# Kernel optimization log

Hardware: AMD Instinct MI355X
Metric: run time of the kernel (lower is better)

The kernel has to match this reference:

```python
import jax, jax.numpy as jnp
import numpy as np

N_HEAD = 16
N_KV_GROUP = 4
WINDOW = 256


def setup_inputs() -> dict:
    key = jax.random.key(0)
    ks = jax.random.split(key, 5)
    B, T, C = 2, 2048, 1024
    KV = C // N_HEAD * N_KV_GROUP  # 256
    s = 0.02
    return {
        "x": jax.random.normal(ks[0], (B, T, C), jnp.float32),
        "Wq": jax.random.normal(ks[1], (C, C), jnp.float32) * s,
        "bq": jnp.zeros((C,), jnp.float32),
        "Wk": jax.random.normal(ks[2], (C, KV), jnp.float32) * s,
        "bk": jnp.zeros((KV,), jnp.float32),
        "Wv": jax.random.normal(ks[3], (C, KV), jnp.float32) * s,
        "bv": jnp.zeros((KV,), jnp.float32),
        "Wo": jax.random.normal(ks[4], (C, C), jnp.float32) * s,
        "bo": jnp.zeros((C,), jnp.float32),
    }


def reference(x, Wq, bq, Wk, bk, Wv, bv, Wo, bo):
    B, T, C = x.shape
    hd = C // N_HEAD  # head dim = 64
    n_rep = N_HEAD // N_KV_GROUP

    q = x @ Wq + bq                      # [B,T,C]
    k = x @ Wk + bk                      # [B,T,KV]
    v = x @ Wv + bv

    q = q.reshape(B, T, N_HEAD, hd).transpose(0, 2, 1, 3)       # [B,H,T,d]
    k = k.reshape(B, T, N_KV_GROUP, hd).transpose(0, 2, 1, 3)   # [B,G,T,d]
    v = v.reshape(B, T, N_KV_GROUP, hd).transpose(0, 2, 1, 3)

    # GQA: repeat_interleave kv heads along head dim
    k_rep = jnp.repeat(k, n_rep, axis=1)                         # [B,H,T,d]
    v_rep = jnp.repeat(v, n_rep, axis=1)

    att = jnp.einsum("bhqd,bhkd->bhqk", q, k_rep) / jnp.sqrt(jnp.float32(hd))

    # causal + sliding window band mask: q position i attends to j in [i-WINDOW, i]
    i = jnp.arange(T)[:, None]
    j = jnp.arange(T)[None, :]
    band = (j <= i) & (j >= i - WINDOW)                           # [T,T]
    att = jnp.where(band[None, None], att, jnp.float32(-jnp.inf))

    att = jax.nn.softmax(att, axis=-1)
    y = jnp.einsum("bhqk,bhkd->bhqd", att, v_rep)                 # [B,H,T,d]
    y = y.transpose(0, 2, 1, 3).reshape(B, T, C)
    return y @ Wo + bo
```

## Files before the change

### kernel.cpp

```cpp
#include <hip/hip_runtime.h>
#include <hip/hip_bf16.h>

#define TT 2048
#define CC 1024
#define KVD 256
#define QKVD 1536

typedef __bf16 bf16x8 __attribute__((ext_vector_type(8)));
typedef float f32x4 __attribute__((ext_vector_type(4)));

__device__ __forceinline__ void gload_lds16(const __hip_bfloat16* g, __hip_bfloat16* l) {
  __builtin_amdgcn_global_load_lds(
      (const __attribute__((address_space(1))) unsigned int*)g,
      (__attribute__((address_space(3))) unsigned int*)l, 16, 0, 0);
}


__global__ __launch_bounds__(256) void k_prep(const float* __restrict__ x,
                                              const float* __restrict__ Wq,
                                              const float* __restrict__ Wk,
                                              const float* __restrict__ Wv,
                                              const float* __restrict__ Wo,
                                              const float* __restrict__ bq,
                                              const float* __restrict__ bk,
                                              const float* __restrict__ bv,
                                              __hip_bfloat16* __restrict__ xbf,
                                              __hip_bfloat16* __restrict__ wqkvT,
                                              __hip_bfloat16* __restrict__ woT,
                                              float* __restrict__ bqkv) {
  const int bxid = blockIdx.x;
  if (bxid < 4096) {
    size_t idx = ((size_t)bxid * 256 + threadIdx.x) * 4;
    float4 v = *(const float4*)(x + idx);
    xbf[idx + 0] = __float2bfloat16(v.x);
    xbf[idx + 1] = __float2bfloat16(v.y);
    xbf[idx + 2] = __float2bfloat16(v.z);
    xbf[idx + 3] = __float2bfloat16(v.w);
    return;
  }
  if (bxid == 4736) {
    for (int i = threadIdx.x; i < 1536; i += 256) {
      float v;
      if (i < 1024)      v = bq[i];
      else if (i < 1280) v = bk[i - 1024];
      else               v = bv[i - 1280];
      bqkv[i] = v;
    }
    return;
  }
  __shared__ float tile[64][65];
  const float* src;
  int ncols, k0, n0;
  __hip_bfloat16* dst;
  if (bxid < 4480) {
    const int idx = bxid - 4096;
    k0 = (idx & 15) * 64;
    n0 = (idx >> 4) * 64;
    dst = wqkvT;
    if (n0 < 1024)      { src = Wq; ncols = 1024; }
    else if (n0 < 1280) { src = Wk - 1024; ncols = 256; }
    else                { src = Wv - 1280; ncols = 256; }
  } else {
    const int idx = bxid - 4480;
    k0 = (idx & 15) * 64;
    n0 = (idx >> 4) * 64;
    dst = woT; src = Wo; ncols = 1024;
  }
  const int rw = threadIdx.x >> 6;
  const int cl = threadIdx.x & 63;
#pragma unroll
  for (int i = 0; i < 16; ++i) {
    const int kr = rw + i * 4;
    tile[kr][cl] = src[(size_t)(k0 + kr) * ncols + n0 + cl];
  }
  __syncthreads();
#pragma unroll
  for (int i = 0; i < 16; ++i) {
    const int nr = rw + i * 4;
    dst[(size_t)(n0 + nr) * 1024 + k0 + cl] = __float2bfloat16(tile[cl][nr]);
  }
}


__global__ __launch_bounds__(512, 4) void k_gemm1(const __hip_bfloat16* __restrict__ A,
                                                  const __hip_bfloat16* __restrict__ BT,
                                                  const float* __restrict__ bias,
                                                  __hip_bfloat16* __restrict__ C,
                                                  __hip_bfloat16* __restrict__ vtg) {
  __shared__ __hip_bfloat16 As[128][64];
  __shared__ __hip_bfloat16 Bs[128][64];

  const int tid  = threadIdx.x;
  const int m0   = blockIdx.y * 128;
  const int n0   = blockIdx.x * 128;
  const int w    = tid >> 6;
  const int lane = tid & 63;
  const int quad = lane >> 4;
  const int l16  = lane & 15;
  const int wm   = (w & 3) * 32;
  const int wn   = (w >> 2) * 64;

  const int dl_r = lane >> 3;
  const int dl_c = (lane & 7) ^ dl_r;

  const __hip_bfloat16* gA = A + (size_t)(m0 + w * 16 + dl_r) * 1024 + dl_c * 8;
  const __hip_bfloat16* gB = BT + (size_t)(n0 + w * 16 + dl_r) * 1024 + dl_c * 8;

  f32x4 acc[2][4] = {};

  for (int kt = 0; kt < 16; ++kt) {
    const int k0 = kt << 6;
    gload_lds16(gA + k0,                    &As[w * 16][0]);
    gload_lds16(gA + k0 + (size_t)8 * 1024, &As[w * 16 + 8][0]);
    gload_lds16(gB + k0,                    &Bs[w * 16][0]);
    gload_lds16(gB + k0 + (size_t)8 * 1024, &Bs[w * 16 + 8][0]);
    __syncthreads();

#pragma unroll
    for (int ks = 0; ks < 2; ++ks) {
      const int cb = (ks << 2) + quad;
      bf16x8 fa[2], fb[4];
#pragma unroll
      for (int i = 0; i < 2; ++i)
        fa[i] = *(const bf16x8*)&As[wm + i * 16 + l16][(cb ^ (l16 & 7)) << 3];
#pragma unroll
      for (int j = 0; j < 4; ++j)
        fb[j] = *(const bf16x8*)&Bs[wn + j * 16 + l16][(cb ^ (l16 & 7)) << 3];
#pragma unroll
      for (int i = 0; i < 2; ++i)
#pragma unroll
        for (int j = 0; j < 4; ++j)
          acc[i][j] = __builtin_amdgcn_mfma_f32_16x16x32_bf16(fa[i], fb[j], acc[i][j], 0, 0, 0);
    }
    __syncthreads();
  }

#pragma unroll
  for (int j = 0; j < 4; ++j) {
    const int gn = n0 + wn + j * 16 + l16;
    const float bias_v = bias[gn];
    if (gn >= 1280) {
      const int dfull = gn - 1280;
      const int gg = dfull >> 6;
      const int dd = dfull & 63;
#pragma unroll
      for (int i = 0; i < 2; ++i) {
        const int gm = m0 + wm + i * 16 + quad * 4;
        const int bb = gm >> 11;
        const int tl = gm & 2047;
        __hip_bfloat16 tmp[4];
#pragma unroll
        for (int r = 0; r < 4; ++r) tmp[r] = __float2bfloat16(acc[i][j][r] + bias_v);
        *(uint2*)(vtg + ((size_t)((bb * 4 + gg) * 64 + dd)) * TT + tl) = *(const uint2*)tmp;
      }
    } else {
#pragma unroll
      for (int i = 0; i < 2; ++i) {
        const int gmb = m0 + wm + i * 16 + quad * 4;
#pragma unroll
        for (int r = 0; r < 4; ++r)
          C[(size_t)(gmb + r) * QKVD + gn] = __float2bfloat16(acc[i][j][r] + bias_v);
      }
    }
  }
}


__global__ __launch_bounds__(256, 4) void k_gemm2(const __hip_bfloat16* __restrict__ A,
                                                  const __hip_bfloat16* __restrict__ BT,
                                                  const float* __restrict__ bias,
                                                  float* __restrict__ C) {
  __shared__ __hip_bfloat16 As[64][64];
  __shared__ __hip_bfloat16 Bs[128][64];

  const int tid  = threadIdx.x;
  const int m0   = blockIdx.y * 64;
  const int n0   = blockIdx.x * 128;
  const int w    = tid >> 6;
  const int lane = tid & 63;
  const int quad = lane >> 4;
  const int l16  = lane & 15;
  const int wm   = (w >> 1) * 32;
  const int wn   = (w & 1) * 64;

  const int dl_r = lane >> 3;
  const int dl_c = (lane & 7) ^ dl_r;

  const __hip_bfloat16* gA = A + (size_t)(m0 + w * 16 + dl_r) * 1024 + dl_c * 8;
  const __hip_bfloat16* gB = BT + (size_t)(n0 + w * 32 + dl_r) * 1024 + dl_c * 8;

  f32x4 acc[2][4] = {};

  for (int kt = 0; kt < 16; ++kt) {
    const int k0 = kt << 6;
    gload_lds16(gA + k0,                     &As[w * 16][0]);
    gload_lds16(gA + k0 + (size_t)8 * 1024,  &As[w * 16 + 8][0]);
    gload_lds16(gB + k0,                     &Bs[w * 32][0]);
    gload_lds16(gB + k0 + (size_t)8 * 1024,  &Bs[w * 32 + 8][0]);
    gload_lds16(gB + k0 + (size_t)16 * 1024, &Bs[w * 32 + 16][0]);
    gload_lds16(gB + k0 + (size_t)24 * 1024, &Bs[w * 32 + 24][0]);
    __syncthreads();

#pragma unroll
    for (int ks = 0; ks < 2; ++ks) {
      const int cb = (ks << 2) + quad;
      bf16x8 fa[2], fb[4];
#pragma unroll
      for (int i = 0; i < 2; ++i)
        fa[i] = *(const bf16x8*)&As[wm + i * 16 + l16][(cb ^ (l16 & 7)) << 3];
#pragma unroll
      for (int j = 0; j < 4; ++j)
        fb[j] = *(const bf16x8*)&Bs[wn + j * 16 + l16][(cb ^ (l16 & 7)) << 3];
#pragma unroll
      for (int i = 0; i < 2; ++i)
#pragma unroll
        for (int j = 0; j < 4; ++j)
          acc[i][j] = __builtin_amdgcn_mfma_f32_16x16x32_bf16(fa[i], fb[j], acc[i][j], 0, 0, 0);
    }
    __syncthreads();
  }

#pragma unroll
  for (int j = 0; j < 4; ++j) {
    const int gn = n0 + wn + j * 16 + l16;
    const float bias_v = bias[gn];
#pragma unroll
    for (int i = 0; i < 2; ++i) {
      const int gmb = m0 + wm + i * 16 + quad * 4;
#pragma unroll
      for (int r = 0; r < 4; ++r)
        C[(size_t)(gmb + r) * CC + gn] = acc[i][j][r] + bias_v;
    }
  }
}


__global__ __launch_bounds__(512) void k_attn(const __hip_bfloat16* __restrict__ qkv,
                                              const __hip_bfloat16* __restrict__ vtg,
                                              __hip_bfloat16* __restrict__ y) {
  __shared__ __hip_bfloat16 Kb[2][64][64];
  __shared__ __hip_bfloat16 Vb[2][64][64];
  __shared__ __hip_bfloat16 Ps[8][16][72];

  const int t    = threadIdx.x;
  const int w    = t >> 6;
  const int lane = t & 63;
  const int quad = lane >> 4;
  const int l16  = lane & 15;
  const int bx   = blockIdx.x;
  const int h    = blockIdx.y;
  const int b    = blockIdx.z;
  const int g    = h >> 2;
  const int i0   = bx * 128;
  const int wg   = w >> 2;
  const int myq0 = i0 + w * 16;
  const int qrow      = myq0 + l16;
  const int my_q_base = myq0 + quad * 4;

  const int lrow = lane >> 3;
  const int cgl  = (lane & 7) ^ lrow;

  const __hip_bfloat16* kg =
      qkv + ((size_t)(b * TT + w * 8 + lrow)) * QKVD + 1024 + g * 64 + cgl * 8;
  const __hip_bfloat16* vg =
      vtg + ((size_t)((b * 4 + g) * 64 + w * 8 + lrow)) * TT + cgl * 8;

  bf16x8 fq[2];
  {
    const __hip_bfloat16* qp = qkv + ((size_t)(b * TT + qrow)) * QKVD + h * 64 + quad * 8;
    fq[0] = *(const bf16x8*)qp;
    fq[1] = *(const bf16x8*)(qp + 32);
  }

  float l_r[4] = {0.f, 0.f, 0.f, 0.f};
  f32x4 o_acc[4] = {};
  const float EC = 0.125f * 1.44269504f;

  const int cc_lo = bx >= 2 ? 0 : (4 - 2 * bx);
  const int jbase = i0 - 256;

  {
    const int jc = jbase + cc_lo * 64;
    gload_lds16(kg + (size_t)jc * QKVD, &Kb[0][w * 8][0]);
    gload_lds16(vg + jc,                &Vb[0][w * 8][0]);
  }

  int buf = 0;
  for (int cc = cc_lo; cc < 6; ++cc) {
    __syncthreads();
    if (cc < 5) {
      const int jn = jbase + (cc + 1) * 64;
      gload_lds16(kg + (size_t)jn * QKVD, &Kb[buf ^ 1][w * 8][0]);
      gload_lds16(vg + jn,                &Vb[buf ^ 1][w * 8][0]);
    }

    if (cc >= wg && cc <= 4 + wg) {
      const int jc = jbase + cc * 64;

      f32x4 sacc[4] = {};
#pragma unroll
      for (int ks = 0; ks < 2; ++ks) {
        const int sw = (((ks << 2) + quad) ^ (l16 & 7)) << 3;
#pragma unroll
        for (int nt = 0; nt < 4; ++nt) {
          const bf16x8 fk = *(const bf16x8*)&Kb[buf][nt * 16 + l16][sw];
          sacc[nt] = __builtin_amdgcn_mfma_f32_16x16x32_bf16(fq[ks], fk, sacc[nt], 0, 0, 0);
        }
      }

      if (cc == 4 + wg) {
#pragma unroll
        for (int r = 0; r < 4; ++r) {
          const int gi = my_q_base + r;
#pragma unroll
          for (int nt = 0; nt < 4; ++nt) {
            const int key = jc + nt * 16 + l16;
            const float p = (key <= gi) ? exp2f(sacc[nt][r] * EC) : 0.f;
            l_r[r] += p;
            Ps[w][quad * 4 + r][nt * 16 + l16] = __float2bfloat16(p);
          }
        }
      } else if (cc == wg) {
#pragma unroll
        for (int r = 0; r < 4; ++r) {
          const int glo = my_q_base + r - 256;
#pragma unroll
          for (int nt = 0; nt < 4; ++nt) {
            const int key = jc + nt * 16 + l16;
            const float p = (key >= glo) ? exp2f(sacc[nt][r] * EC) : 0.f;
            l_r[r] += p;
            Ps[w][quad * 4 + r][nt * 16 + l16] = __float2bfloat16(p);
          }
        }
      } else {
#pragma unroll
        for (int r = 0; r < 4; ++r)
#pragma unroll
          for (int nt = 0; nt < 4; ++nt) {
            const float p = exp2f(sacc[nt][r] * EC);
            l_r[r] += p;
            Ps[w][quad * 4 + r][nt * 16 + l16] = __float2bfloat16(p);
          }
      }

      const bf16x8 fp0 = *(const bf16x8*)&Ps[w][l16][quad * 8];
      const bf16x8 fp1 = *(const bf16x8*)&Ps[w][l16][32 + quad * 8];

#pragma unroll
      for (int ks = 0; ks < 2; ++ks) {
        const int sw = (((ks << 2) + quad) ^ (l16 & 7)) << 3;
#pragma unroll
        for (int jt = 0; jt < 4; ++jt) {
          const bf16x8 fv = *(const bf16x8*)&Vb[buf][jt * 16 + l16][sw];
          o_acc[jt] = __builtin_amdgcn_mfma_f32_16x16x32_bf16(ks == 0 ? fp0 : fp1, fv,
                                                              o_acc[jt], 0, 0, 0);
        }
      }
    }
    buf ^= 1;
  }

#pragma unroll
  for (int r = 0; r < 4; ++r) {
#pragma unroll
    for (int d = 1; d < 16; d <<= 1) l_r[r] += __shfl_xor(l_r[r], d);
    const float inv = 1.f / l_r[r];
    __hip_bfloat16* yp = y + ((size_t)(b * TT + my_q_base + r)) * CC + h * 64 + l16;
#pragma unroll
    for (int jt = 0; jt < 4; ++jt)
      yp[jt * 16] = __float2bfloat16(o_acc[jt][r] * inv);
  }
}


extern "C" void kernel_launch(void* const* d_in, const int* in_sizes, int n_in,
                              void* d_out, int out_size, void* d_ws, size_t ws_size,
                              hipStream_t stream) {
  const float* x  = (const float*)d_in[0];
  const float* Wq = (const float*)d_in[1];
  const float* bq = (const float*)d_in[2];
  const float* Wk = (const float*)d_in[3];
  const float* bk = (const float*)d_in[4];
  const float* Wv = (const float*)d_in[5];
  const float* bv = (const float*)d_in[6];
  const float* Wo = (const float*)d_in[7];
  const float* bo = (const float*)d_in[8];
  float* out = (float*)d_out;

  char* ws = (char*)d_ws;
  const size_t M = 2 * TT;
  __hip_bfloat16* xbf   = (__hip_bfloat16*)(ws);
  __hip_bfloat16* qkv   = (__hip_bfloat16*)(ws + 8388608);
  __hip_bfloat16* ybf   = (__hip_bfloat16*)(ws + 20971520);
  __hip_bfloat16* wqkvT = (__hip_bfloat16*)(ws + 29360128);
  __hip_bfloat16* woT   = (__hip_bfloat16*)(ws + 32505856);
  float*          bqkv  = (float*)(ws + 34603008);
  __hip_bfloat16* vtg   = (__hip_bfloat16*)(ws + 34609152);

  k_prep<<<4737, 256, 0, stream>>>(x, Wq, Wk, Wv, Wo, bq, bk, bv,
                                   xbf, wqkvT, woT, bqkv);

  k_gemm1<<<dim3(QKVD / 128, M / 128), 512, 0, stream>>>(xbf, wqkvT, bqkv, qkv, vtg);

  k_attn<<<dim3(TT / 128, 16, 2), 512, 0, stream>>>(qkv, vtg, ybf);

  k_gemm2<<<dim3(CC / 128, M / 64), 256, 0, stream>>>(ybf, woT, bo, out);
}
```

Measured before the change: 142.5 us.

## Double-buffer LDS tiles in both projection GEMMs to overlap loads with MFMA

Both bf16 GEMM kernels now use two LDS buffers per operand and prefetch the next K tile via global_load_lds while MFMAs run on the current tile, removing one barrier per iteration. This is meant to hide global memory latency behind compute. LDS usage per block doubles and the launch-bound occupancy hints are lowered, which reduces the number of resident blocks that could otherwise hide latency.

Result: slower. 148.6 us (+4.3%).

```diff
diff --git a/kernel.cpp b/kernel.cpp
--- a/kernel.cpp
+++ b/kernel.cpp
@@ -82,13 +82,13 @@
 }
 
 
-__global__ __launch_bounds__(512, 4) void k_gemm1(const __hip_bfloat16* __restrict__ A,
+__global__ __launch_bounds__(512, 2) void k_gemm1(const __hip_bfloat16* __restrict__ A,
                                                   const __hip_bfloat16* __restrict__ BT,
                                                   const float* __restrict__ bias,
                                                   __hip_bfloat16* __restrict__ C,
                                                   __hip_bfloat16* __restrict__ vtg) {
-  __shared__ __hip_bfloat16 As[128][64];
-  __shared__ __hip_bfloat16 Bs[128][64];
+  __shared__ __hip_bfloat16 As[2][128][64];
+  __shared__ __hip_bfloat16 Bs[2][128][64];
 
   const int tid  = threadIdx.x;
   const int m0   = blockIdx.y * 128;
@@ -108,13 +108,21 @@
 
   f32x4 acc[2][4] = {};
 
+  gload_lds16(gA,                    &As[0][w * 16][0]);
+  gload_lds16(gA + (size_t)8 * 1024, &As[0][w * 16 + 8][0]);
+  gload_lds16(gB,                    &Bs[0][w * 16][0]);
+  gload_lds16(gB + (size_t)8 * 1024, &Bs[0][w * 16 + 8][0]);
+
+  int buf = 0;
   for (int kt = 0; kt < 16; ++kt) {
-    const int k0 = kt << 6;
-    gload_lds16(gA + k0,                    &As[w * 16][0]);
-    gload_lds16(gA + k0 + (size_t)8 * 1024, &As[w * 16 + 8][0]);
-    gload_lds16(gB + k0,                    &Bs[w * 16][0]);
-    gload_lds16(gB + k0 + (size_t)8 * 1024, &Bs[w * 16 + 8][0]);
     __syncthreads();
+    if (kt < 15) {
+      const int kn = (kt + 1) << 6;
+      gload_lds16(gA + kn,                    &As[buf ^ 1][w * 16][0]);
+      gload_lds16(gA + kn + (size_t)8 * 1024, &As[buf ^ 1][w * 16 + 8][0]);
+      gload_lds16(gB + kn,                    &Bs[buf ^ 1][w * 16][0]);
+      gload_lds16(gB + kn + (size_t)8 * 1024, &Bs[buf ^ 1][w * 16 + 8][0]);
+    }
 
 #pragma unroll
     for (int ks = 0; ks < 2; ++ks) {
@@ -122,17 +130,17 @@
       bf16x8 fa[2], fb[4];
 #pragma unroll
       for (int i = 0; i < 2; ++i)
-        fa[i] = *(const bf16x8*)&As[wm + i * 16 + l16][(cb ^ (l16 & 7)) << 3];
+        fa[i] = *(const bf16x8*)&As[buf][wm + i * 16 + l16][(cb ^ (l16 & 7)) << 3];
 #pragma unroll
       for (int j = 0; j < 4; ++j)
-        fb[j] = *(const bf16x8*)&Bs[wn + j * 16 + l16][(cb ^ (l16 & 7)) << 3];
+        fb[j] = *(const bf16x8*)&Bs[buf][wn + j * 16 + l16][(cb ^ (l16 & 7)) << 3];
 #pragma unroll
       for (int i = 0; i < 2; ++i)
 #pragma unroll
         for (int j = 0; j < 4; ++j)
           acc[i][j] = __builtin_amdgcn_mfma_f32_16x16x32_bf16(fa[i], fb[j], acc[i][j], 0, 0, 0);
     }
-    __syncthreads();
+    buf ^= 1;
   }
 
 #pragma unroll
@@ -166,12 +174,12 @@
 }
 
 
-__global__ __launch_bounds__(256, 4) void k_gemm2(const __hip_bfloat16* __restrict__ A,
+__global__ __launch_bounds__(256, 3) void k_gemm2(const __hip_bfloat16* __restrict__ A,
                                                   const __hip_bfloat16* __restrict__ BT,
                                                   const float* __restrict__ bias,
                                                   float* __restrict__ C) {
-  __shared__ __hip_bfloat16 As[64][64];
-  __shared__ __hip_bfloat16 Bs[128][64];
+  __shared__ __hip_bfloat16 As[2][64][64];
+  __shared__ __hip_bfloat16 Bs[2][128][64];
 
   const int tid  = threadIdx.x;
   const int m0   = blockIdx.y * 64;
@@ -191,15 +199,25 @@
 
   f32x4 acc[2][4] = {};
 
+  gload_lds16(gA,                     &As[0][w * 16][0]);
+  gload_lds16(gA + (size_t)8 * 1024,  &As[0][w * 16 + 8][0]);
+  gload_lds16(gB,                     &Bs[0][w * 32][0]);
+  gload_lds16(gB + (size_t)8 * 1024,  &Bs[0][w * 32 + 8][0]);
+  gload_lds16(gB + (size_t)16 * 1024, &Bs[0][w * 32 + 16][0]);
+  gload_lds16(gB + (size_t)24 * 1024, &Bs[0][w * 32 + 24][0]);
+
+  int buf = 0;
   for (int kt = 0; kt < 16; ++kt) {
-    const int k0 = kt << 6;
-    gload_lds16(gA + k0,                     &As[w * 16][0]);
-    gload_lds16(gA + k0 + (size_t)8 * 1024,  &As[w * 16 + 8][0]);
-    gload_lds16(gB + k0,                     &Bs[w * 32][0]);
-    gload_lds16(gB + k0 + (size_t)8 * 1024,  &Bs[w * 32 + 8][0]);
-    gload_lds16(gB + k0 + (size_t)16 * 1024, &Bs[w * 32 + 16][0]);
-    gload_lds16(gB + k0 + (size_t)24 * 1024, &Bs[w * 32 + 24][0]);
     __syncthreads();
+    if (kt < 15) {
+      const int kn = (kt + 1) << 6;
+      gload_lds16(gA + kn,                     &As[buf ^ 1][w * 16][0]);
+      gload_lds16(gA + kn + (size_t)8 * 1024,  &As[buf ^ 1][w * 16 + 8][0]);
+      gload_lds16(gB + kn,                     &Bs[buf ^ 1][w * 32][0]);
+      gload_lds16(gB + kn + (size_t)8 * 1024,  &Bs[buf ^ 1][w * 32 + 8][0]);
+      gload_lds16(gB + kn + (size_t)16 * 1024, &Bs[buf ^ 1][w * 32 + 16][0]);
+      gload_lds16(gB + kn + (size_t)24 * 1024, &Bs[buf ^ 1][w * 32 + 24][0]);
+    }
 
 #pragma unroll
     for (int ks = 0; ks < 2; ++ks) {
@@ -207,17 +225,17 @@
       bf16x8 fa[2], fb[4];
 #pragma unroll
       for (int i = 0; i < 2; ++i)
-        fa[i] = *(const bf16x8*)&As[wm + i * 16 + l16][(cb ^ (l16 & 7)) << 3];
+        fa[i] = *(const bf16x8*)&As[buf][wm + i * 16 + l16][(cb ^ (l16 & 7)) << 3];
 #pragma unroll
       for (int j = 0; j < 4; ++j)
-        fb[j] = *(const bf16x8*)&Bs[wn + j * 16 + l16][(cb ^ (l16 & 7)) << 3];
+        fb[j] = *(const bf16x8*)&Bs[buf][wn + j * 16 + l16][(cb ^ (l16 & 7)) << 3];
 #pragma unroll
       for (int i = 0; i < 2; ++i)
 #pragma unroll
         for (int j = 0; j < 4; ++j)
           acc[i][j] = __builtin_amdgcn_mfma_f32_16x16x32_bf16(fa[i], fb[j], acc[i][j], 0, 0, 0);
     }
-    __syncthreads();
+    buf ^= 1;
   }
 
 #pragma unroll
```
